# Kernel optimization log

Hardware: AMD Instinct MI355X
Metric: run time of the kernel (lower is better)

## Reference

```python
import jax, jax.numpy as jnp
import numpy as np

N_NODES, N_EDGES, F_IN, DIM, N_CLASSES, N_GRAPHS, N_RUNS, N_LAYERS = 20000, 320000, 64, 64, 16, 128, 4, 4
BN_EPS = 1e-5


def setup_inputs() -> dict:
    key = jax.random.key(0)
    ks = jax.random.split(key, 20)
    inp = {}
    inp["x"] = jax.random.normal(ks[0], (N_NODES, F_IN), dtype=jnp.float32)
    inp["edge_index"] = jax.random.randint(ks[1], (2, N_EDGES), 0, N_NODES)
    inp["batch"] = jnp.sort(jax.random.randint(ks[2], (N_NODES,), 0, N_GRAPHS))
    inp["drop_mask"] = jax.random.randint(ks[3], (N_RUNS, N_NODES), 0, 2).astype(bool)
    s = 0.05
    L, D, C = N_LAYERS, DIM, N_CLASSES
    inp["convW1"] = jax.random.normal(ks[4], (L, D, D), dtype=jnp.float32) * s  # layer0 in-dim == F_IN == DIM
    inp["convb1"] = jnp.zeros((L, D), jnp.float32)
    inp["mlp_bn_g"] = jnp.ones((L, D), jnp.float32)
    inp["mlp_bn_b"] = jnp.zeros((L, D), jnp.float32)
    inp["convW2"] = jax.random.normal(ks[5], (L, D, D), dtype=jnp.float32) * s
    inp["convb2"] = jnp.zeros((L, D), jnp.float32)
    inp["bn_g"] = jnp.ones((L, D), jnp.float32)
    inp["bn_b"] = jnp.zeros((L, D), jnp.float32)
    inp["fcW"] = jax.random.normal(ks[6], (L + 1, D, C), dtype=jnp.float32) * s
    inp["fcb"] = jnp.zeros((L + 1, C), jnp.float32)
    return inp


def _bn(z, g, b):
    # BatchNorm1d in training mode: stats over all (run, node) rows, biased var
    m = z.mean(axis=(0, 1))
    v = jnp.mean(jnp.square(z - m), axis=(0, 1))
    return (z - m) * jax.lax.rsqrt(v + BN_EPS) * g + b


def reference(x, edge_index, batch, drop_mask, convW1, convb1, mlp_bn_g, mlp_bn_b,
              convW2, convb2, bn_g, bn_b, fcW, fcb):
    R = drop_mask.shape[0]
    N = x.shape[0]
    src, dst = edge_index[0], edge_index[1]
    # node dropout per run
    h = jnp.where(drop_mask[:, :, None], 0.0, jnp.broadcast_to(x, (R,) + x.shape))  # [R,N,F]
    outs = [h]
    for i in range(N_LAYERS):
        # GINConv (eps=0): mlp(x + sum_{j in N(i)} x_j), scatter-add over edges per run
        agg = jax.vmap(lambda hr: jax.ops.segment_sum(hr[src], dst, num_segments=N))(h)
        z = h + agg
        z = jnp.einsum("rnd,de->rne", z, convW1[i]) + convb1[i]
        z = jax.nn.relu(_bn(z, mlp_bn_g[i], mlp_bn_b[i]))
        z = jnp.einsum("rnd,de->rne", z, convW2[i]) + convb2[i]
        h = jax.nn.relu(_bn(z, bn_g[i], bn_b[i]))
        outs.append(h)
    out = jnp.zeros((N_GRAPHS, fcW.shape[-1]), x.dtype)
    for i, o in enumerate(outs):
        m = o.mean(axis=0)  # mean over runs -> [N,D]
        pooled = jax.ops.segment_sum(m, batch, num_segments=N_GRAPHS)  # global_add_pool
        out = out + pooled @ fcW[i] + fcb[i]  # dropout inactive in eval
    return jax.nn.log_softmax(out, axis=-1)
```

## Files before the change

### kernel.cpp

```cpp
#include <hip/hip_runtime.h>

typedef unsigned short u16;
typedef unsigned int u32;
typedef __attribute__((ext_vector_type(8))) short bf16x8;
typedef __attribute__((ext_vector_type(4))) float f32x4;

#define NN 20000
#define NE 320000
#define NPAD 20032
#define D 64
#define R 4
#define NG 128
#define NC 16
#define NL 4
#define MROWS (NN*R)
#define NBLKF (NPAD/8)
#define NBLKG (NPAD/16)
#define NPART NBLKF
#define NPOOL (4*NG)
#define EPAD 480256
#define BN_EPS 1e-5f

__device__ __forceinline__ float bf2f(u16 v) {
    union { u32 u; float f; } c; c.u = ((u32)v) << 16; return c.f;
}
__device__ __forceinline__ u16 f2bf(float f) {
    union { u32 u; float f; } c; c.f = f;
    u32 u = c.u;
    return (u16)((u + 0x7fffu + ((u >> 16) & 1u)) >> 16);
}
__device__ __forceinline__ int swz(int row, int kbyte) {
    return row * 64 + (((kbyte) ^ ((row & 7) << 4)) >> 1);
}

__global__ void k_setup(const float* __restrict__ x, const int* __restrict__ mask,
                        u16* __restrict__ H, int* __restrict__ esrc, int* __restrict__ deg,
                        float* __restrict__ pooled) {
    int id = blockIdx.x * 256 + threadIdx.x;
    if (id < EPAD) esrc[id] = NN;
    if (id < NPAD) deg[id] = 0;
    if (id < 5 * NG * 64) pooled[id] = 0.f;
    if (id < NPAD * 64) {
        int n = id >> 6, r = (id >> 4) & 3, q = id & 15;
        ushort4 o; o.x = o.y = o.z = o.w = 0;
        if (n < NN && mask[r * NN + n] == 0) {
            float4 v = *(const float4*)(x + (size_t)n * 64 + q * 4);
            o.x = f2bf(v.x); o.y = f2bf(v.y); o.z = f2bf(v.z); o.w = f2bf(v.w);
        }
        *(ushort4*)(H + ((size_t)n * 4 + r) * 64 + q * 4) = o;
    }
}

__global__ void k_deg(const int* __restrict__ dst, int* __restrict__ deg) {
    int e = blockIdx.x * 256 + threadIdx.x;
    if (e < NE) atomicAdd(&deg[dst[e]], 1);
}

__global__ __launch_bounds__(1024) void k_scan(const int* __restrict__ deg,
                                               int* __restrict__ rowstart,
                                               int* __restrict__ cursor,
                                               int* __restrict__ esrc) {
    __shared__ int wsum[16];
    __shared__ int woff[16];
    __shared__ int carry_s, chunktot;
    const int t = threadIdx.x, lane = t & 63, wv = t >> 6;
    if (t == 0) carry_s = 0;
    __syncthreads();
    for (int base = 0; base < NPAD; base += 1024) {
        int i = base + t;
        int v = (i < NN) ? ((deg[i] + 4) & ~3) : 0;
        int x = v;
#pragma unroll
        for (int off = 1; off < 64; off <<= 1) {
            int y = __shfl_up(x, off);
            if (lane >= off) x += y;
        }
        if (lane == 63) wsum[wv] = x;
        __syncthreads();
        if (t < 16) {
            int s = wsum[t], sx = s;
#pragma unroll
            for (int off = 1; off < 16; off <<= 1) {
                int y = __shfl_up(sx, off);
                if (t >= off) sx += y;
            }
            woff[t] = sx - s;
            if (t == 15) chunktot = sx;
        }
        __syncthreads();
        int excl = carry_s + woff[wv] + x - v;
        if (i < NPAD) rowstart[i] = excl;
        if (i < NN) { esrc[excl] = i; cursor[i] = excl + 1; }
        __syncthreads();
        if (t == 0) carry_s += chunktot;
        __syncthreads();
    }
    if (t == 0) rowstart[NPAD] = carry_s;
}

__global__ void k_fill(const int* __restrict__ src, const int* __restrict__ dst,
                       int* __restrict__ cursor, int* __restrict__ esrc) {
    int e = blockIdx.x * 256 + threadIdx.x;
    if (e < NE) {
        int p = atomicAdd(&cursor[dst[e]], 1);
        esrc[p] = src[e];
    }
}

__global__ __launch_bounds__(256) void k_fgg(const u16* __restrict__ Z,
                                             u16* __restrict__ Y,
                                             const int* __restrict__ rowstart,
                                             const int* __restrict__ esrc,
                                             const float* __restrict__ W,
                                             const float* __restrict__ bias,
                                             float* __restrict__ part) {
    __shared__ __align__(16) u16 Xs[32 * 64];
    __shared__ __align__(16) u16 Wt[64 * 64];
    __shared__ float red[128];
    const int t = threadIdx.x, lane = t & 63, wv = t >> 6;
    const int blk = blockIdx.x;
    const int node0 = blk * 8;

    {
        int k = t >> 2, cb = (t & 3) * 16;
        const float* Wp = W + k * 64 + cb;
        float4 v0 = *(const float4*)Wp;
        float4 v1 = *(const float4*)(Wp + 4);
        float4 v2 = *(const float4*)(Wp + 8);
        float4 v3 = *(const float4*)(Wp + 12);
        float vv[16] = {v0.x, v0.y, v0.z, v0.w, v1.x, v1.y, v1.z, v1.w,
                        v2.x, v2.y, v2.z, v2.w, v3.x, v3.y, v3.z, v3.w};
#pragma unroll
        for (int j = 0; j < 16; j++) Wt[swz(cb + j, k * 2)] = f2bf(vv[j]);
    }

    const int rr = lane >> 4, cl = (lane & 15) * 4;
#pragma unroll
    for (int i = 0; i < 2; i++) {
        const int n = node0 + wv * 2 + i;
        float a0 = 0.f, a1 = 0.f, a2 = 0.f, a3 = 0.f;
        int s0 = __builtin_amdgcn_readfirstlane(rowstart[n]);
        int s1 = __builtin_amdgcn_readfirstlane(rowstart[n + 1]);
#define ACC(v) { a0 += bf2f(v.x); a1 += bf2f(v.y); a2 += bf2f(v.z); a3 += bf2f(v.w); }
        int k = s0;
        for (; k + 8 <= s1; k += 8) {
            int4 ia = *(const int4*)(esrc + k);
            int4 ib = *(const int4*)(esrc + k + 4);
            ushort4 w0 = *(const ushort4*)(Z + (size_t)ia.x * 256 + lane * 4);
            ushort4 w1 = *(const ushort4*)(Z + (size_t)ia.y * 256 + lane * 4);
            ushort4 w2 = *(const ushort4*)(Z + (size_t)ia.z * 256 + lane * 4);
            ushort4 w3 = *(const ushort4*)(Z + (size_t)ia.w * 256 + lane * 4);
            ushort4 w4 = *(const ushort4*)(Z + (size_t)ib.x * 256 + lane * 4);
            ushort4 w5 = *(const ushort4*)(Z + (size_t)ib.y * 256 + lane * 4);
            ushort4 w6 = *(const ushort4*)(Z + (size_t)ib.z * 256 + lane * 4);
            ushort4 w7 = *(const ushort4*)(Z + (size_t)ib.w * 256 + lane * 4);
            ACC(w0) ACC(w1) ACC(w2) ACC(w3) ACC(w4) ACC(w5) ACC(w6) ACC(w7)
        }
        if (k < s1) {
            int4 ia = *(const int4*)(esrc + k);
            ushort4 w0 = *(const ushort4*)(Z + (size_t)ia.x * 256 + lane * 4);
            ushort4 w1 = *(const ushort4*)(Z + (size_t)ia.y * 256 + lane * 4);
            ushort4 w2 = *(const ushort4*)(Z + (size_t)ia.z * 256 + lane * 4);
            ushort4 w3 = *(const ushort4*)(Z + (size_t)ia.w * 256 + lane * 4);
            ACC(w0) ACC(w1) ACC(w2) ACC(w3)
        }
#undef ACC
        const int lrow = (wv * 2 + i) * 4 + rr;
        u32 lo = (u32)f2bf(a0) | ((u32)f2bf(a1) << 16);
        u32 hi = (u32)f2bf(a2) | ((u32)f2bf(a3) << 16);
        *(uint2*)&Xs[swz(lrow, cl * 2)] = make_uint2(lo, hi);
    }
    __syncthreads();

    const int l15 = lane & 15, l4 = lane >> 4;
    const int col = wv * 16 + l15;
    bf16x8 a00 = *(bf16x8*)&Xs[swz(l15, l4 * 16)];
    bf16x8 a01 = *(bf16x8*)&Xs[swz(l15, 64 + l4 * 16)];
    bf16x8 a10 = *(bf16x8*)&Xs[swz(16 + l15, l4 * 16)];
    bf16x8 a11 = *(bf16x8*)&Xs[swz(16 + l15, 64 + l4 * 16)];
    bf16x8 bf0 = *(bf16x8*)&Wt[swz(col, l4 * 16)];
    bf16x8 bf1 = *(bf16x8*)&Wt[swz(col, 64 + l4 * 16)];
    float bv = bias[col];
    f32x4 acc0 = (f32x4){bv, bv, bv, bv};
    f32x4 acc1 = acc0;
    acc0 = __builtin_amdgcn_mfma_f32_16x16x32_bf16(a00, bf0, acc0, 0, 0, 0);
    acc0 = __builtin_amdgcn_mfma_f32_16x16x32_bf16(a01, bf1, acc0, 0, 0, 0);
    acc1 = __builtin_amdgcn_mfma_f32_16x16x32_bf16(a10, bf0, acc1, 0, 0, 0);
    acc1 = __builtin_amdgcn_mfma_f32_16x16x32_bf16(a11, bf1, acc1, 0, 0, 0);

    const size_t ybase = (size_t)node0 * 4 * 64;
    float s = 0.f, q = 0.f;
#pragma unroll
    for (int j = 0; j < 4; j++) {
        int row0 = l4 * 4 + j, row1 = 16 + l4 * 4 + j;
        Y[ybase + (size_t)row0 * 64 + col] = f2bf(acc0[j]);
        Y[ybase + (size_t)row1 * 64 + col] = f2bf(acc1[j]);
        float m0 = (node0 + (row0 >> 2) < NN) ? 1.f : 0.f;
        float m1 = (node0 + (row1 >> 2) < NN) ? 1.f : 0.f;
        float v0 = m0 * acc0[j], v1 = m1 * acc1[j];
        s += v0 + v1;
        q += v0 * acc0[j] + v1 * acc1[j];
    }
    s += __shfl_xor(s, 16); s += __shfl_xor(s, 32);
    q += __shfl_xor(q, 16); q += __shfl_xor(q, 32);
    if (l4 == 0) {
        red[wv * 32 + l15] = s;
        red[wv * 32 + 16 + l15] = q;
    }
    __syncthreads();
    if (t < 128) {
        int c = (t < 64) ? t : (t - 64);
        int off = (t < 64) ? 0 : 16;
        part[(size_t)t * NPART + blk] = red[(c >> 4) * 32 + off + (c & 15)];
    }
}

__global__ __launch_bounds__(256) void k_gemm(const u16* __restrict__ Pin,
                                              u16* __restrict__ Qout,
                                              const float* __restrict__ W,
                                              const float* __restrict__ bias,
                                              const float* __restrict__ inStats,
                                              const float* __restrict__ gamma,
                                              const float* __restrict__ beta,
                                              float* __restrict__ part) {
    __shared__ __align__(16) u16 Xs[64 * 64];
    __shared__ __align__(16) u16 Wt[64 * 64];
    __shared__ float red[512];
    __shared__ float Psc[64], Psh[64];
    const int t = threadIdx.x, lane = t & 63, wv = t >> 6;
    const int blk = blockIdx.x;
    const int m0 = blk * 64;

    {
        int k = t >> 2, cb = (t & 3) * 16;
        const float* Wp = W + k * 64 + cb;
        float4 v0 = *(const float4*)Wp;
        float4 v1 = *(const float4*)(Wp + 4);
        float4 v2 = *(const float4*)(Wp + 8);
        float4 v3 = *(const float4*)(Wp + 12);
        float vv[16] = {v0.x, v0.y, v0.z, v0.w, v1.x, v1.y, v1.z, v1.w,
                        v2.x, v2.y, v2.z, v2.w, v3.x, v3.y, v3.z, v3.w};
#pragma unroll
        for (int j = 0; j < 16; j++) Wt[swz(cb + j, k * 2)] = f2bf(vv[j]);
    }
    if (t < 64) {
        float m = inStats[t] * (1.0f / MROWS);
        float var = inStats[64 + t] * (1.0f / MROWS) - m * m;
        float sc = gamma[t] * rsqrtf(var + BN_EPS);
        Psc[t] = sc;
        Psh[t] = beta[t] - m * sc;
    }
    __syncthreads();

    const int row = t >> 2, cb = (t & 3) * 16;
    const size_t base = (size_t)m0 * 64;
    {
        const u16* Xp = Pin + base + (size_t)row * 64 + cb;
        uint4 a = *(const uint4*)Xp;
        uint4 bq = *(const uint4*)(Xp + 8);
        u32 w[8] = {a.x, a.y, a.z, a.w, bq.x, bq.y, bq.z, bq.w};
        u32 ow[8];
#pragma unroll
        for (int j = 0; j < 8; j++) {
            int c = cb + 2 * j;
            union { u32 u; float f; } lo, hi;
            lo.u = w[j] << 16;
            hi.u = w[j] & 0xffff0000u;
            float v0 = fmaxf(fmaf(lo.f, Psc[c], Psh[c]), 0.f);
            float v1 = fmaxf(fmaf(hi.f, Psc[c + 1], Psh[c + 1]), 0.f);
            ow[j] = (u32)f2bf(v0) | ((u32)f2bf(v1) << 16);
        }
        *(uint4*)&Xs[swz(row, cb * 2)] = make_uint4(ow[0], ow[1], ow[2], ow[3]);
        *(uint4*)&Xs[swz(row, cb * 2 + 16)] = make_uint4(ow[4], ow[5], ow[6], ow[7]);
    }
    __syncthreads();

    const int l4 = lane >> 4, l15 = lane & 15;
    const int arow = wv * 16 + l15;
    bf16x8 af0 = *(bf16x8*)&Xs[swz(arow, l4 * 16)];
    bf16x8 af1 = *(bf16x8*)&Xs[swz(arow, 64 + l4 * 16)];
    f32x4 acc[4];
#pragma unroll
    for (int n0 = 0; n0 < 4; n0++) {
        int n = n0 * 16 + l15;
        float bv = bias[n];
        acc[n0] = (f32x4){bv, bv, bv, bv};
        bf16x8 bf0 = *(bf16x8*)&Wt[swz(n, l4 * 16)];
        bf16x8 bf1 = *(bf16x8*)&Wt[swz(n, 64 + l4 * 16)];
        acc[n0] = __builtin_amdgcn_mfma_f32_16x16x32_bf16(af0, bf0, acc[n0], 0, 0, 0);
        acc[n0] = __builtin_amdgcn_mfma_f32_16x16x32_bf16(af1, bf1, acc[n0], 0, 0, 0);
    }

#pragma unroll
    for (int n0 = 0; n0 < 4; n0++) {
        int col = n0 * 16 + l15;
#pragma unroll
        for (int j = 0; j < 4; j++) {
            int lrow = wv * 16 + l4 * 4 + j;
            Qout[base + (size_t)lrow * 64 + col] = f2bf(acc[n0][j]);
        }
    }

#pragma unroll
    for (int n0 = 0; n0 < 4; n0++) {
        float s = 0.f, q = 0.f;
#pragma unroll
        for (int j = 0; j < 4; j++) {
            int lrow = wv * 16 + l4 * 4 + j;
            float vm = (((m0 + lrow) >> 2) < NN) ? 1.f : 0.f;
            float v = vm * acc[n0][j];
            s += v; q += v * acc[n0][j];
        }
        s += __shfl_xor(s, 16); s += __shfl_xor(s, 32);
        q += __shfl_xor(q, 16); q += __shfl_xor(q, 32);
        if (l4 == 0) {
            red[wv * 128 + n0 * 16 + l15] = s;
            red[wv * 128 + 64 + n0 * 16 + l15] = q;
        }
    }
    __syncthreads();
    if (t < 128) {
        float v = red[t] + red[128 + t] + red[256 + t] + red[384 + t];
        part[(size_t)t * NPART + blk] = v;
    }
}

__global__ __launch_bounds__(256) void k_statreduce(const float* __restrict__ part,
                                                    float* __restrict__ stats, int count) {
    const int j = blockIdx.x, t = threadIdx.x;
    float s = 0.f;
    for (int p = t; p < count; p += 256) s += part[(size_t)j * NPART + p];
#pragma unroll
    for (int off = 32; off > 0; off >>= 1) s += __shfl_xor(s, off);
    __shared__ float red[4];
    if ((t & 63) == 0) red[t >> 6] = s;
    __syncthreads();
    if (t == 0) stats[j] = red[0] + red[1] + red[2] + red[3];
}

template <bool APPLY>
__global__ __launch_bounds__(256) void k_pool(const u16* __restrict__ Zin,
                                              const int* __restrict__ batch,
                                              float* __restrict__ pooled,
                                              u16* __restrict__ Hout,
                                              const float* __restrict__ stats,
                                              const float* __restrict__ g,
                                              const float* __restrict__ b) {
    const int blk = blockIdx.x;
    const int gr = blk >> 2, r = blk & 3;
    const int t = threadIdx.x, lane = t & 63, wv = t >> 6;
    int lo = 0, hi = NN;
    while (lo < hi) { int mid = (lo + hi) >> 1; if (batch[mid] < gr) lo = mid + 1; else hi = mid; }
    const int start = lo;
    lo = 0; hi = NN;
    while (lo < hi) { int mid = (lo + hi) >> 1; if (batch[mid] < gr + 1) lo = mid + 1; else hi = mid; }
    const int end = lo;

    float sc = 1.f, sh = 0.f;
    if (APPLY) {
        float m = stats[lane] * (1.f / MROWS);
        float var = stats[64 + lane] * (1.f / MROWS) - m * m;
        sc = g[lane] * rsqrtf(var + BN_EPS);
        sh = b[lane] - m * sc;
    }
    float acc = 0.f;
#define PBODY(nn)                                                              \
    {                                                                          \
        float f = bf2f(Zin[((size_t)(nn) * 4 + r) * 64 + lane]);               \
        if (APPLY) {                                                           \
            f = fmaxf(fmaf(f, sc, sh), 0.f);                                   \
            Hout[((size_t)(nn) * 4 + r) * 64 + lane] = f2bf(f);                \
        }                                                                      \
        acc += f;                                                              \
    }
    int n = start + wv;
    for (; n + 12 < end; n += 16) { PBODY(n); PBODY(n + 4); PBODY(n + 8); PBODY(n + 12); }
    for (; n < end; n += 4) PBODY(n);
#undef PBODY
    __shared__ float red[4][64];
    red[wv][lane] = acc;
    __syncthreads();
    if (t < 64) {
        float s = red[0][t] + red[1][t] + red[2][t] + red[3][t];
        atomicAdd(&pooled[gr * 64 + t], 0.25f * s);
    }
}

__global__ __launch_bounds__(256) void k_readout(const float* __restrict__ pooled,
                                                 const float* __restrict__ fcW,
                                                 const float* __restrict__ fcb,
                                                 float* __restrict__ out) {
    const int gr = blockIdx.x, t = threadIdx.x;
    const int c = t & 15, seg = t >> 4;
    float acc = 0.f;
#pragma unroll
    for (int i = 0; i < 5; i++)
#pragma unroll
        for (int k = 0; k < 4; k++) {
            int d = seg * 4 + k;
            acc = fmaf(pooled[i * (NG * D) + gr * D + d], fcW[i * 1024 + d * 16 + c], acc);
        }
    __shared__ float red[16][17];
    red[seg][c] = acc;
    __syncthreads();
    if (t < 16) {
        float s = 0.f;
#pragma unroll
        for (int s2 = 0; s2 < 16; s2++) s += red[s2][t];
#pragma unroll
        for (int i = 0; i < 5; i++) s += fcb[i * NC + t];
        float mx = s;
#pragma unroll
        for (int m = 1; m < 16; m <<= 1) mx = fmaxf(mx, __shfl_xor(mx, m));
        float e = expf(s - mx), se = e;
#pragma unroll
        for (int m = 1; m < 16; m <<= 1) se += __shfl_xor(se, m);
        out[gr * NC + t] = s - mx - logf(se);
    }
}

extern "C" void kernel_launch(void* const* d_in, const int* in_sizes, int n_in,
                              void* d_out, int out_size, void* d_ws, size_t ws_size,
                              hipStream_t stream) {
    const float* x = (const float*)d_in[0];
    const int* ei = (const int*)d_in[1];
    const int* srcp = ei;
    const int* dstp = ei + NE;
    const int* batch = (const int*)d_in[2];
    const int* mask = (const int*)d_in[3];
    const float* convW1 = (const float*)d_in[4];
    const float* convb1 = (const float*)d_in[5];
    const float* mlp_bn_g = (const float*)d_in[6];
    const float* mlp_bn_b = (const float*)d_in[7];
    const float* convW2 = (const float*)d_in[8];
    const float* convb2 = (const float*)d_in[9];
    const float* bn_g = (const float*)d_in[10];
    const float* bn_b = (const float*)d_in[11];
    const float* fcW = (const float*)d_in[12];
    const float* fcb = (const float*)d_in[13];
    float* out = (float*)d_out;

    u16* H = (u16*)d_ws;
    u16* P = H + (size_t)NPAD * 256;
    u16* Q = P + (size_t)NPAD * 256;
    float* pooled = (float*)(Q + (size_t)NPAD * 256);
    float* stats = pooled + 5 * NG * D;
    float* part = stats + NL * 2 * 128;
    int* rowstart = (int*)(part + 128 * NPART);
    int* cursor = rowstart + NPAD + 1;
    int* deg = cursor + NPAD;
    int* esrc = deg + NPAD;

    k_setup<<<(NPAD * 64 + 255) / 256, 256, 0, stream>>>(x, mask, H, esrc, deg, pooled);
    k_deg<<<(NE + 255) / 256, 256, 0, stream>>>(dstp, deg);
    k_scan<<<1, 1024, 0, stream>>>(deg, rowstart, cursor, esrc);
    k_fill<<<(NE + 255) / 256, 256, 0, stream>>>(srcp, dstp, cursor, esrc);

    k_pool<false><<<NPOOL, 256, 0, stream>>>(H, batch, pooled, nullptr,
                                             nullptr, nullptr, nullptr);

    for (int i = 0; i < NL; i++) {
        float* st1 = stats + (i * 2 + 0) * 128;
        float* st2 = stats + (i * 2 + 1) * 128;
        k_fgg<<<NBLKF, 256, 0, stream>>>(H, P, rowstart, esrc,
                                         convW1 + i * 4096, convb1 + i * 64, part);
        k_statreduce<<<128, 256, 0, stream>>>(part, st1, NBLKF);
        k_gemm<<<NBLKG, 256, 0, stream>>>(P, Q, convW2 + i * 4096, convb2 + i * 64,
                                          st1, mlp_bn_g + i * 64, mlp_bn_b + i * 64, part);
        k_statreduce<<<128, 256, 0, stream>>>(part, st2, NBLKG);
        k_pool<true><<<NPOOL, 256, 0, stream>>>(Q, batch, pooled + (i + 1) * (NG * D), H,
                                                st2, bn_g + i * 64, bn_b + i * 64);
    }

    k_readout<<<NG, 256, 0, stream>>>(pooled, fcW, fcb, out);
}
```

Baseline: 311.0 us.

## Switch activations to run-major layout with XCD-aware run assignment in gather

```diff
diff --git a/kernel.cpp b/kernel.cpp
--- a/kernel.cpp
+++ b/kernel.cpp
@@ -14,8 +14,10 @@
 #define NC 16
 #define NL 4
 #define MROWS (NN*R)
-#define NBLKF (NPAD/8)
-#define NBLKG (NPAD/16)
+#define NTILE (NPAD/32)
+#define HTILE (NTILE/2)
+#define NBLKF (R*NTILE)
+#define NBLKG (R*NPAD/64)
 #define NPART NBLKF
 #define NPOOL (4*NG)
 #define EPAD 480256
@@ -40,14 +42,16 @@
     if (id < EPAD) esrc[id] = NN;
     if (id < NPAD) deg[id] = 0;
     if (id < 5 * NG * 64) pooled[id] = 0.f;
-    if (id < NPAD * 64) {
-        int n = id >> 6, r = (id >> 4) & 3, q = id & 15;
+    if (id < R * NPAD * 16) {
+        int r = id / (NPAD * 16);
+        int rem = id - r * (NPAD * 16);
+        int n = rem >> 4, q = rem & 15;
         ushort4 o; o.x = o.y = o.z = o.w = 0;
         if (n < NN && mask[r * NN + n] == 0) {
             float4 v = *(const float4*)(x + (size_t)n * 64 + q * 4);
             o.x = f2bf(v.x); o.y = f2bf(v.y); o.z = f2bf(v.z); o.w = f2bf(v.w);
         }
-        *(ushort4*)(H + ((size_t)n * 4 + r) * 64 + q * 4) = o;
+        *(ushort4*)(H + ((size_t)r * NPAD + n) * 64 + q * 4) = o;
     }
 }
 
@@ -119,7 +123,10 @@
     __shared__ float red[128];
     const int t = threadIdx.x, lane = t & 63, wv = t >> 6;
     const int blk = blockIdx.x;
-    const int node0 = blk * 8;
+    const int xcd = blk & 7;
+    const int run = xcd & 3;
+    const int node0 = ((blk >> 3) + HTILE * (xcd >> 2)) * 32;
+    const u16* Zr = Z + (size_t)run * (NPAD * 64);
 
     {
         int k = t >> 2, cb = (t & 3) * 16;
@@ -134,41 +141,37 @@
         for (int j = 0; j < 16; j++) Wt[swz(cb + j, k * 2)] = f2bf(vv[j]);
     }
 
-    const int rr = lane >> 4, cl = (lane & 15) * 4;
-#pragma unroll
-    for (int i = 0; i < 2; i++) {
-        const int n = node0 + wv * 2 + i;
+    const int g = lane >> 4, cl = (lane & 15) * 4;
+    for (int i = 0; i < 8; i++) {
+        const int n = node0 + wv * 8 + i;
         float a0 = 0.f, a1 = 0.f, a2 = 0.f, a3 = 0.f;
         int s0 = __builtin_amdgcn_readfirstlane(rowstart[n]);
         int s1 = __builtin_amdgcn_readfirstlane(rowstart[n + 1]);
 #define ACC(v) { a0 += bf2f(v.x); a1 += bf2f(v.y); a2 += bf2f(v.z); a3 += bf2f(v.w); }
         int k = s0;
         for (; k + 8 <= s1; k += 8) {
-            int4 ia = *(const int4*)(esrc + k);
-            int4 ib = *(const int4*)(esrc + k + 4);
-            ushort4 w0 = *(const ushort4*)(Z + (size_t)ia.x * 256 + lane * 4);
-            ushort4 w1 = *(const ushort4*)(Z + (size_t)ia.y * 256 + lane * 4);
-            ushort4 w2 = *(const ushort4*)(Z + (size_t)ia.z * 256 + lane * 4);
-            ushort4 w3 = *(const ushort4*)(Z + (size_t)ia.w * 256 + lane * 4);
-            ushort4 w4 = *(const ushort4*)(Z + (size_t)ib.x * 256 + lane * 4);
-            ushort4 w5 = *(const ushort4*)(Z + (size_t)ib.y * 256 + lane * 4);
-            ushort4 w6 = *(const ushort4*)(Z + (size_t)ib.z * 256 + lane * 4);
-            ushort4 w7 = *(const ushort4*)(Z + (size_t)ib.w * 256 + lane * 4);
-            ACC(w0) ACC(w1) ACC(w2) ACC(w3) ACC(w4) ACC(w5) ACC(w6) ACC(w7)
+            int e0 = esrc[k + g];
+            int e1 = esrc[k + 4 + g];
+            ushort4 va = *(const ushort4*)(Zr + (size_t)e0 * 64 + cl);
+            ushort4 vb = *(const ushort4*)(Zr + (size_t)e1 * 64 + cl);
+            ACC(va) ACC(vb)
         }
         if (k < s1) {
-            int4 ia = *(const int4*)(esrc + k);
-            ushort4 w0 = *(const ushort4*)(Z + (size_t)ia.x * 256 + lane * 4);
-            ushort4 w1 = *(const ushort4*)(Z + (size_t)ia.y * 256 + lane * 4);
-            ushort4 w2 = *(const ushort4*)(Z + (size_t)ia.z * 256 + lane * 4);
-            ushort4 w3 = *(const ushort4*)(Z + (size_t)ia.w * 256 + lane * 4);
-            ACC(w0) ACC(w1) ACC(w2) ACC(w3)
+            int e0 = esrc[k + g];
+            ushort4 va = *(const ushort4*)(Zr + (size_t)e0 * 64 + cl);
+            ACC(va)
         }
 #undef ACC
-        const int lrow = (wv * 2 + i) * 4 + rr;
-        u32 lo = (u32)f2bf(a0) | ((u32)f2bf(a1) << 16);
-        u32 hi = (u32)f2bf(a2) | ((u32)f2bf(a3) << 16);
-        *(uint2*)&Xs[swz(lrow, cl * 2)] = make_uint2(lo, hi);
+        a0 += __shfl_xor(a0, 16); a0 += __shfl_xor(a0, 32);
+        a1 += __shfl_xor(a1, 16); a1 += __shfl_xor(a1, 32);
+        a2 += __shfl_xor(a2, 16); a2 += __shfl_xor(a2, 32);
+        a3 += __shfl_xor(a3, 16); a3 += __shfl_xor(a3, 32);
+        if (g == 0) {
+            const int lrow = wv * 8 + i;
+            u32 lo = (u32)f2bf(a0) | ((u32)f2bf(a1) << 16);
+            u32 hi = (u32)f2bf(a2) | ((u32)f2bf(a3) << 16);
+            *(uint2*)&Xs[swz(lrow, cl * 2)] = make_uint2(lo, hi);
+        }
     }
     __syncthreads();
 
@@ -188,15 +191,15 @@
     acc1 = __builtin_amdgcn_mfma_f32_16x16x32_bf16(a10, bf0, acc1, 0, 0, 0);
     acc1 = __builtin_amdgcn_mfma_f32_16x16x32_bf16(a11, bf1, acc1, 0, 0, 0);
 
-    const size_t ybase = (size_t)node0 * 4 * 64;
+    const size_t ybase = ((size_t)run * NPAD + node0) * 64;
     float s = 0.f, q = 0.f;
 #pragma unroll
     for (int j = 0; j < 4; j++) {
         int row0 = l4 * 4 + j, row1 = 16 + l4 * 4 + j;
-        Y[ybase + (size_t)row0 * 64 + col] = f2bf(acc0[j]);
-        Y[ybase + (size_t)row1 * 64 + col] = f2bf(acc1[j]);
-        float m0 = (node0 + (row0 >> 2) < NN) ? 1.f : 0.f;
-        float m1 = (node0 + (row1 >> 2) < NN) ? 1.f : 0.f;
+        __builtin_nontemporal_store(f2bf(acc0[j]), &Y[ybase + (size_t)row0 * 64 + col]);
+        __builtin_nontemporal_store(f2bf(acc1[j]), &Y[ybase + (size_t)row1 * 64 + col]);
+        float m0 = (node0 + row0 < NN) ? 1.f : 0.f;
+        float m1 = (node0 + row1 < NN) ? 1.f : 0.f;
         float v0 = m0 * acc0[j], v1 = m1 * acc1[j];
         s += v0 + v1;
         q += v0 * acc0[j] + v1 * acc1[j];
@@ -229,7 +232,8 @@
     __shared__ float Psc[64], Psh[64];
     const int t = threadIdx.x, lane = t & 63, wv = t >> 6;
     const int blk = blockIdx.x;
-    const int m0 = blk * 64;
+    const int rblk = blk / (NPAD / 64);
+    const int n0 = (blk % (NPAD / 64)) * 64;
 
     {
         int k = t >> 2, cb = (t & 3) * 16;
@@ -253,7 +257,7 @@
     __syncthreads();
 
     const int row = t >> 2, cb = (t & 3) * 16;
-    const size_t base = (size_t)m0 * 64;
+    const size_t base = ((size_t)rblk * NPAD + n0) * 64;
     {
         const u16* Xp = Pin + base + (size_t)row * 64 + cb;
         uint4 a = *(const uint4*)Xp;
@@ -281,41 +285,42 @@
     bf16x8 af1 = *(bf16x8*)&Xs[swz(arow, 64 + l4 * 16)];
     f32x4 acc[4];
 #pragma unroll
-    for (int n0 = 0; n0 < 4; n0++) {
-        int n = n0 * 16 + l15;
+    for (int nb = 0; nb < 4; nb++) {
+        int n = nb * 16 + l15;
         float bv = bias[n];
-        acc[n0] = (f32x4){bv, bv, bv, bv};
+        acc[nb] = (f32x4){bv, bv, bv, bv};
         bf16x8 bf0 = *(bf16x8*)&Wt[swz(n, l4 * 16)];
         bf16x8 bf1 = *(bf16x8*)&Wt[swz(n, 64 + l4 * 16)];
-        acc[n0] = __builtin_amdgcn_mfma_f32_16x16x32_bf16(af0, bf0, acc[n0], 0, 0, 0);
-        acc[n0] = __builtin_amdgcn_mfma_f32_16x16x32_bf16(af1, bf1, acc[n0], 0, 0, 0);
-    }
-
-#pragma unroll
-    for (int n0 = 0; n0 < 4; n0++) {
-        int col = n0 * 16 + l15;
+        acc[nb] = __builtin_amdgcn_mfma_f32_16x16x32_bf16(af0, bf0, acc[nb], 0, 0, 0);
+        acc[nb] = __builtin_amdgcn_mfma_f32_16x16x32_bf16(af1, bf1, acc[nb], 0, 0, 0);
+    }
+
+#pragma unroll
+    for (int nb = 0; nb < 4; nb++) {
+        int col = nb * 16 + l15;
 #pragma unroll
         for (int j = 0; j < 4; j++) {
             int lrow = wv * 16 + l4 * 4 + j;
-            Qout[base + (size_t)lrow * 64 + col] = f2bf(acc[n0][j]);
-        }
-    }
-
-#pragma unroll
-    for (int n0 = 0; n0 < 4; n0++) {
+            __builtin_nontemporal_store(f2bf(acc[nb][j]),
+                                        &Qout[base + (size_t)lrow * 64 + col]);
+        }
+    }
+
+#pragma unroll
+    for (int nb = 0; nb < 4; nb++) {
         float s = 0.f, q = 0.f;
 #pragma unroll
         for (int j = 0; j < 4; j++) {
             int lrow = wv * 16 + l4 * 4 + j;
-            float vm = (((m0 + lrow) >> 2) < NN) ? 1.f : 0.f;
-            float v = vm * acc[n0][j];
-            s += v; q += v * acc[n0][j];
+            float vm = (n0 + lrow < NN) ? 1.f : 0.f;
+            float v = vm * acc[nb][j];
+            s += v; q += v * acc[nb][j];
         }
         s += __shfl_xor(s, 16); s += __shfl_xor(s, 32);
         q += __shfl_xor(q, 16); q += __shfl_xor(q, 32);
         if (l4 == 0) {
-            red[wv * 128 + n0 * 16 + l15] = s;
-            red[wv * 128 + 64 + n0 * 16 + l15] = q;
+            red[wv * 128 + nb * 16 + l15] = s;
+            red[wv * 128 + 64 + nb * 16 + l15] = q;
         }
     }
     __syncthreads();
@@ -348,7 +353,7 @@
                                               const float* __restrict__ b) {
     const int blk = blockIdx.x;
     const int gr = blk >> 2, r = blk & 3;
-    const int t = threadIdx.x, lane = t & 63, wv = t >> 6;
+    const int t = threadIdx.x;
     int lo = 0, hi = NN;
     while (lo < hi) { int mid = (lo + hi) >> 1; if (batch[mid] < gr) lo = mid + 1; else hi = mid; }
     const int start = lo;
@@ -356,32 +361,52 @@
     while (lo < hi) { int mid = (lo + hi) >> 1; if (batch[mid] < gr + 1) lo = mid + 1; else hi = mid; }
     const int end = lo;
 
-    float sc = 1.f, sh = 0.f;
+    const int grp = t >> 4;
+    const int cl = (t & 15) * 4;
+    const u16* Zr = Zin + (size_t)r * (NPAD * 64);
+    u16* Hr = Hout + (size_t)r * (NPAD * 64);
+    float sc[4], sh[4];
     if (APPLY) {
-        float m = stats[lane] * (1.f / MROWS);
-        float var = stats[64 + lane] * (1.f / MROWS) - m * m;
-        sc = g[lane] * rsqrtf(var + BN_EPS);
-        sh = b[lane] - m * sc;
-    }
-    float acc = 0.f;
+#pragma unroll
+        for (int j = 0; j < 4; j++) {
+            int c = cl + j;
+            float m = stats[c] * (1.f / MROWS);
+            float var = stats[64 + c] * (1.f / MROWS) - m * m;
+            float s = g[c] * rsqrtf(var + BN_EPS);
+            sc[j] = s;
+            sh[j] = b[c] - m * s;
+        }
+    }
+    float a0 = 0.f, a1 = 0.f, a2 = 0.f, a3 = 0.f;
 #define PBODY(nn)                                                              \
     {                                                                          \
-        float f = bf2f(Zin[((size_t)(nn) * 4 + r) * 64 + lane]);               \
+        ushort4 v = *(const ushort4*)(Zr + (size_t)(nn) * 64 + cl);            \
+        float f0 = bf2f(v.x), f1 = bf2f(v.y), f2 = bf2f(v.z), f3 = bf2f(v.w);  \
         if (APPLY) {                                                           \
-            f = fmaxf(fmaf(f, sc, sh), 0.f);                                   \
-            Hout[((size_t)(nn) * 4 + r) * 64 + lane] = f2bf(f);                \
+            f0 = fmaxf(fmaf(f0, sc[0], sh[0]), 0.f);                           \
+            f1 = fmaxf(fmaf(f1, sc[1], sh[1]), 0.f);                           \
+            f2 = fmaxf(fmaf(f2, sc[2], sh[2]), 0.f);                           \
+            f3 = fmaxf(fmaf(f3, sc[3], sh[3]), 0.f);                           \
+            ushort4 o;                                                         \
+            o.x = f2bf(f0); o.y = f2bf(f1); o.z = f2bf(f2); o.w = f2bf(f3);    \
+            *(ushort4*)(Hr + (size_t)(nn) * 64 + cl) = o;                      \
         }                                                                      \
-        acc += f;                                                              \
-    }
-    int n = start + wv;
-    for (; n + 12 < end; n += 16) { PBODY(n); PBODY(n + 4); PBODY(n + 8); PBODY(n + 12); }
-    for (; n < end; n += 4) PBODY(n);
+        a0 += f0; a1 += f1; a2 += f2; a3 += f3;                                \
+    }
+    int n = start + grp;
+    for (; n + 16 < end; n += 32) { PBODY(n); PBODY(n + 16); }
+    for (; n < end; n += 16) PBODY(n);
 #undef PBODY
-    __shared__ float red[4][64];
-    red[wv][lane] = acc;
+    __shared__ float red[16 * 64];
+    red[grp * 64 + cl + 0] = a0;
+    red[grp * 64 + cl + 1] = a1;
+    red[grp * 64 + cl + 2] = a2;
+    red[grp * 64 + cl + 3] = a3;
     __syncthreads();
     if (t < 64) {
-        float s = red[0][t] + red[1][t] + red[2][t] + red[3][t];
+        float s = 0.f;
+#pragma unroll
+        for (int k = 0; k < 16; k++) s += red[k * 64 + t];
         atomicAdd(&pooled[gr * 64 + t], 0.25f * s);
     }
 }
@@ -441,9 +466,9 @@
     float* out = (float*)d_out;
 
     u16* H = (u16*)d_ws;
-    u16* P = H + (size_t)NPAD * 256;
-    u16* Q = P + (size_t)NPAD * 256;
-    float* pooled = (float*)(Q + (size_t)NPAD * 256);
+    u16* P = H + (size_t)R * NPAD * 64;
+    u16* Q = P + (size_t)R * NPAD * 64;
+    float* pooled = (float*)(Q + (size_t)R * NPAD * 64);
     float* stats = pooled + 5 * NG * D;
     float* part = stats + NL * 2 * 128;
     int* rowstart = (int*)(part + 128 * NPART);
@@ -451,7 +476,7 @@
     int* deg = cursor + NPAD;
     int* esrc = deg + NPAD;
 
-    k_setup<<<(NPAD * 64 + 255) / 256, 256, 0, stream>>>(x, mask, H, esrc, deg, pooled);
+    k_setup<<<(R * NPAD * 16 + 255) / 256, 256, 0, stream>>>(x, mask, H, esrc, deg, pooled);
     k_deg<<<(NE + 255) / 256, 256, 0, stream>>>(dstp, deg);
     k_scan<<<1, 1024, 0, stream>>>(deg, rowstart, cursor, esrc);
     k_fill<<<(NE + 255) / 256, 256, 0, stream>>>(srcp, dstp, cursor, esrc);
```

Measured after the change: 355.8 us. 1.14x slower.
